# Optimization experiments

Measured on AMD Instinct MI355X. Metric: run time of the kernel, lower is better.

Reference implementation:

```python
import jax, jax.numpy as jnp
import numpy as np

D_IN = 1024
D_OUT = 1024


def setup_inputs() -> dict:
    key = jax.random.key(0)
    kx, kq, kk, kv = jax.random.split(key, 4)
    x = jax.random.normal(kx, (4, 2048, D_IN), dtype=jnp.float32)
    # nn.Linear weight has shape [d_out, d_in]; y = x @ W.T
    s = 1.0 / np.sqrt(D_IN)
    W_query = jax.random.uniform(kq, (D_OUT, D_IN), jnp.float32, -s, s)
    W_key = jax.random.uniform(kk, (D_OUT, D_IN), jnp.float32, -s, s)
    W_value = jax.random.uniform(kv, (D_OUT, D_IN), jnp.float32, -s, s)
    return {"x": x, "W_query": W_query, "W_key": W_key, "W_value": W_value}


def reference(x, W_query, W_key, W_value):
    # x: [b, n, d_in]; W_*: [d_out, d_in]
    q = jnp.einsum("bnd,kd->bnk", x, W_query)
    k = jnp.einsum("bnd,kd->bnk", x, W_key)
    v = jnp.einsum("bnd,kd->bnk", x, W_value)
    d_k = W_query.shape[0]
    scores = jnp.einsum("bqk,bnk->bqn", q, k) * (d_k ** -0.5)  # [b, n, n]
    weights = jax.nn.softmax(scores, axis=-1)
    return jnp.einsum("bqn,bnk->bqk", weights, v)
```

## Files before the change

kernel.cpp:

```cpp
#include <hip/hip_runtime.h>
#include <hip/hip_bf16.h>
#include <stdint.h>


typedef __attribute__((ext_vector_type(8))) short bf16x8;
typedef __attribute__((ext_vector_type(4))) float f32x4;

__device__ __forceinline__ void async_copy16(const void* g, void* l) {
  __builtin_amdgcn_global_load_lds(
      (__attribute__((address_space(1))) void*)(g),
      (__attribute__((address_space(3))) void*)(l),
      16, 0, 0);
}

__device__ __forceinline__ void mainloop256(
    const __hip_bfloat16* __restrict__ aS,
    const __hip_bfloat16* __restrict__ bS,
    __hip_bfloat16* As, __hip_bfloat16* Bs,
    const int wid, const int wm, const int wn,
    const int l16, const int quad, const int sw,
    f32x4 (&acc)[8][4])
{
  const bf16x8* Av = (const bf16x8*)As;
  const bf16x8* Bv = (const bf16x8*)Bs;
  char* lA = (char*)As + wid * 1024;
  char* lB = (char*)Bs + wid * 1024;
  bf16x8 bfr[4][2];
  bf16x8 afc[2][2], afn[2][2];

#define SB0 __builtin_amdgcn_sched_barrier(0)

#define STG_A2(t) do { \
    async_copy16(aS + ((t)*64 +        0), lA + ((t)&1)*32768 +        0); \
    async_copy16(aS + ((t)*64 +  64*1024), lA + ((t)&1)*32768 +  64*128); \
    async_copy16(aS + ((t)*64 + 128*1024), lA + ((t)&1)*32768 + 128*128); \
    async_copy16(aS + ((t)*64 + 192*1024), lA + ((t)&1)*32768 + 192*128); \
  } while (0)
#define STG_B2(t) do { \
    async_copy16(bS + ((t)*64 +        0), lB + ((t)&1)*32768 +        0); \
    async_copy16(bS + ((t)*64 +  64*1024), lB + ((t)&1)*32768 +  64*128); \
    async_copy16(bS + ((t)*64 + 128*1024), lB + ((t)&1)*32768 + 128*128); \
    async_copy16(bS + ((t)*64 + 192*1024), lB + ((t)&1)*32768 + 192*128); \
  } while (0)

#define RD_AF(dst, t, phi) do { \
    _Pragma("unroll") \
    for (int m2 = 0; m2 < 2; ++m2) \
      _Pragma("unroll") \
      for (int kk = 0; kk < 2; ++kk) \
        dst[m2][kk] = Av[((t)&1)*2048 + (wm + ((phi)*2 + m2)*16 + l16)*8 + ((kk*4 + quad) ^ sw)]; \
  } while (0)
#define RD_BF(t, nlo, nhi) do { \
    _Pragma("unroll") \
    for (int ni = (nlo); ni < (nhi); ++ni) \
      _Pragma("unroll") \
      for (int kk = 0; kk < 2; ++kk) \
        bfr[ni][kk] = Bv[((t)&1)*2048 + (wn + ni*16 + l16)*8 + ((kk*4 + quad) ^ sw)]; \
  } while (0)
#define MM(src, phi, nlo, nhi) do { \
    _Pragma("unroll") \
    for (int kk = 0; kk < 2; ++kk) \
      _Pragma("unroll") \
      for (int m2 = 0; m2 < 2; ++m2) \
        _Pragma("unroll") \
        for (int ni = (nlo); ni < (nhi); ++ni) \
          acc[(phi)*2 + m2][ni] = __builtin_amdgcn_mfma_f32_16x16x32_bf16( \
              src[m2][kk], bfr[ni][kk], acc[(phi)*2 + m2][ni], 0, 0, 0); \
  } while (0)

#define TILE(t, STG0_STMT, STG1_STMT, GATE_STMT) do { \
     \
    RD_BF(t, 0, 2); \
    RD_AF(afc, t, 0); \
    STG0_STMT; \
    asm volatile("s_waitcnt lgkmcnt(0)"); SB0; \
    RD_BF(t, 2, 4); \
    SB0; \
    RD_AF(afn, t, 1); \
    SB0; \
    __builtin_amdgcn_s_setprio(1); MM(afc, 0, 0, 2); __builtin_amdgcn_s_setprio(0); \
    asm volatile("s_waitcnt lgkmcnt(4)"); SB0; \
    __builtin_amdgcn_s_setprio(1); MM(afc, 0, 2, 4); __builtin_amdgcn_s_setprio(0); \
    SB0; \
    __builtin_amdgcn_s_barrier();    \
     \
    STG1_STMT; \
    asm volatile("s_waitcnt lgkmcnt(0)"); SB0; \
    RD_AF(afc, t, 2); \
    SB0; \
    __builtin_amdgcn_s_setprio(1); MM(afn, 1, 0, 4); __builtin_amdgcn_s_setprio(0); \
     \
    asm volatile("s_waitcnt lgkmcnt(0)"); SB0; \
    RD_AF(afn, t, 3); \
    SB0; \
    __builtin_amdgcn_s_setprio(1); MM(afc, 2, 0, 4); __builtin_amdgcn_s_setprio(0); \
     \
    asm volatile("s_waitcnt lgkmcnt(0)"); SB0; \
    __builtin_amdgcn_s_setprio(1); MM(afn, 3, 0, 4); __builtin_amdgcn_s_setprio(0); \
    GATE_STMT; \
    SB0; \
    __builtin_amdgcn_s_barrier(); \
  } while (0)

#define GATE4 asm volatile("s_waitcnt vmcnt(4)")
#define GATE0 asm volatile("s_waitcnt vmcnt(0)")
#define GNONE (void)0

  STG_B2(0); STG_A2(0); STG_B2(1);
  asm volatile("s_waitcnt vmcnt(4)");
  __builtin_amdgcn_s_barrier();

  #pragma unroll 1
  for (int i = 0; i < 7; ++i) {
    const int ta = 2 * i, tb = 2 * i + 1;
    TILE(ta, STG_A2(tb),     STG_B2(ta + 2), GATE4);
    TILE(tb, STG_A2(ta + 2), STG_B2(tb + 2), GATE4);
  }
  TILE(14, STG_A2(15), GNONE, GATE0);
  TILE(15, GNONE,      GNONE, GNONE);

#undef TILE
#undef GATE4
#undef GATE0
#undef GNONE
#undef MM
#undef RD_BF
#undef RD_AF
#undef STG_A2
#undef STG_B2
#undef SB0
}

__global__ __launch_bounds__(512, 2)
void gemm_qkv(const __hip_bfloat16* __restrict__ A,
              const __hip_bfloat16* __restrict__ B,
              __hip_bfloat16* __restrict__ Q,
              __hip_bfloat16* __restrict__ Kk,
              __hip_bfloat16* __restrict__ Vt)
{
  __shared__ __align__(16) __hip_bfloat16 As[2][256 * 64];
  __shared__ __align__(16) __hip_bfloat16 Bs[2][256 * 64];

  const int bid = blockIdx.x;
  const int s   = (bid & 7) * 48 + (bid >> 3);
  const long long tile_m = (long long)(s / 12) * 256;
  const long long tile_n = (long long)(s % 12) * 256;

  const int tid  = threadIdx.x;
  const int wid  = tid >> 6;
  const int lane = tid & 63;
  const int srow = wid * 8 + (lane >> 3);
  const int scol = ((lane & 7) ^ (lane >> 3)) * 8;

  const __hip_bfloat16* aS = A + (tile_m + srow) * 1024 + scol;
  const __hip_bfloat16* bS = B + (tile_n + srow) * 1024 + scol;

  const int wm   = (wid >> 2) * 128;
  const int wn   = (wid & 3) * 64;
  const int quad = lane >> 4;
  const int l16  = lane & 15;
  const int sw   = l16 & 7;

  f32x4 acc[8][4];
  #pragma unroll
  for (int mi = 0; mi < 8; ++mi)
    #pragma unroll
    for (int ni = 0; ni < 4; ++ni)
      acc[mi][ni] = (f32x4){0.f, 0.f, 0.f, 0.f};

  mainloop256(aS, bS, &As[0][0], &Bs[0][0], wid, wm, wn, l16, quad, sw, acc);

  const int mat = (int)(tile_n >> 10);
  if (mat < 2) {
    __hip_bfloat16* outp = (mat == 0) ? Q : Kk;
    const float scale = (mat == 0) ? 0.03125f : 1.0f;
    const int coln0 = (int)(tile_n & 1023);
    #pragma unroll
    for (int mi = 0; mi < 8; ++mi) {
      #pragma unroll
      for (int r = 0; r < 4; ++r) {
        const long long row = tile_m + wm + mi * 16 + quad * 4 + r;
        #pragma unroll
        for (int ni = 0; ni < 4; ++ni) {
          const int col = coln0 + wn + ni * 16 + l16;
          outp[row * 1024 + col] = __float2bfloat16(acc[mi][ni][r] * scale);
        }
      }
    }
  } else {
    const int b    = (int)(tile_m >> 11);
    const int seq0 = (int)(tile_m & 2047);
    const int d0   = (int)(tile_n - 2048);
    #pragma unroll
    for (int mi = 0; mi < 8; ++mi) {
      const int seq = seq0 + wm + mi * 16 + quad * 4;
      #pragma unroll
      for (int ni = 0; ni < 4; ++ni) {
        const int d = d0 + wn + ni * 16 + l16;
        union { ushort4 u; unsigned short sh[4]; } pk;
        #pragma unroll
        for (int r = 0; r < 4; ++r)
          pk.sh[r] = __bfloat16_as_ushort(__float2bfloat16(acc[mi][ni][r]));
        *(ushort4*)(Vt + ((long long)(b * 1024 + d)) * 2048 + seq) = pk.u;
      }
    }
  }
}

__global__ __launch_bounds__(512, 2)
void gemm_s_exp(const __hip_bfloat16* __restrict__ A,
                const __hip_bfloat16* __restrict__ B,
                __hip_bfloat16* __restrict__ Cout,
                float* __restrict__ part)
{
  __shared__ __align__(16) __hip_bfloat16 As[2][256 * 64];
  __shared__ __align__(16) __hip_bfloat16 Bs[2][256 * 64];

  const int bz = blockIdx.z;
  A += (long long)bz * 2048 * 1024;
  B += (long long)bz * 2048 * 1024;

  const long long tile_m = (long long)blockIdx.y * 256;
  const long long tile_n = (long long)blockIdx.x * 256;

  const int tid  = threadIdx.x;
  const int wid  = tid >> 6;
  const int lane = tid & 63;
  const int srow = wid * 8 + (lane >> 3);
  const int scol = ((lane & 7) ^ (lane >> 3)) * 8;

  const __hip_bfloat16* aS = A + (tile_m + srow) * 1024 + scol;
  const __hip_bfloat16* bS = B + (tile_n + srow) * 1024 + scol;

  const int wm   = (wid >> 2) * 128;
  const int wn   = (wid & 3) * 64;
  const int quad = lane >> 4;
  const int l16  = lane & 15;
  const int sw   = l16 & 7;

  f32x4 acc[8][4];
  #pragma unroll
  for (int mi = 0; mi < 8; ++mi)
    #pragma unroll
    for (int ni = 0; ni < 4; ++ni)
      acc[mi][ni] = (f32x4){0.f, 0.f, 0.f, 0.f};

  mainloop256(aS, bS, &As[0][0], &Bs[0][0], wid, wm, wn, l16, quad, sw, acc);

  __hip_bfloat16* C = Cout + (long long)bz * 2048 * 2048;
  #pragma unroll
  for (int mi = 0; mi < 8; ++mi) {
    #pragma unroll
    for (int r = 0; r < 4; ++r) {
      const long long row = tile_m + wm + mi * 16 + quad * 4 + r;
      float ssum = 0.f;
      #pragma unroll
      for (int ni = 0; ni < 4; ++ni) {
        const float e = __expf(acc[mi][ni][r]);
        const __hip_bfloat16 h = __float2bfloat16(e);
        C[row * 2048 + tile_n + wn + ni * 16 + l16] = h;
        ssum += __bfloat162float(h);
      }
      #pragma unroll
      for (int off = 1; off < 16; off <<= 1) ssum += __shfl_xor(ssum, off, 64);
      if (l16 == 0)
        part[((long long)bz * 2048 + row) * 32 + blockIdx.x * 4 + (wid & 3)] = ssum;
    }
  }
}

__global__ __launch_bounds__(256)
void gemm_pv(const __hip_bfloat16* __restrict__ A,
             const __hip_bfloat16* __restrict__ B,
             const float* __restrict__ part,
             float* __restrict__ Cout)
{
  __shared__ __align__(16) __hip_bfloat16 As[128 * 64];
  __shared__ __align__(16) __hip_bfloat16 Bs[128 * 64];
  __shared__ float rinv[128];

  const int K = 2048, N = 1024;
  const int bz = blockIdx.z;
  A += (long long)bz * 2048 * 2048;
  B += (long long)bz * 1024 * 2048;

  const long long tile_m = (long long)blockIdx.y * 128;
  const long long tile_n = (long long)blockIdx.x * 128;

  const int tid  = threadIdx.x;
  const int wid  = tid >> 6;
  const int lane = tid & 63;

  const int srow = wid * 8 + (lane >> 3);
  const int scol = (((lane & 7) ^ (lane >> 3))) * 8;

  const __hip_bfloat16* aptr = A + (tile_m + srow) * K + scol;
  const __hip_bfloat16* bptr = B + (tile_n + srow) * K + scol;
  char* la = (char*)As + (wid * 8) * 128;
  char* lb = (char*)Bs + (wid * 8) * 128;

  const int wm   = (wid >> 1) * 64;
  const int wn   = (wid & 1) * 64;
  const int quad = lane >> 4;
  const int l16  = lane & 15;
  const int sw   = l16 & 7;

  const bf16x8* Asv = (const bf16x8*)As;
  const bf16x8* Bsv = (const bf16x8*)Bs;

  f32x4 acc[4][4];
  #pragma unroll
  for (int mi = 0; mi < 4; ++mi)
    #pragma unroll
    for (int ni = 0; ni < 4; ++ni)
      acc[mi][ni] = (f32x4){0.f, 0.f, 0.f, 0.f};

  for (int k0 = 0; k0 < K; k0 += 64) {
    #pragma unroll
    for (int p = 0; p < 4; ++p)
      async_copy16(aptr + (long long)p * 32 * K, la + p * 32 * 128);
    #pragma unroll
    for (int p = 0; p < 4; ++p)
      async_copy16(bptr + (long long)p * 32 * K, lb + p * 32 * 128);
    aptr += 64;
    bptr += 64;
    __syncthreads();

    #pragma unroll
    for (int kk = 0; kk < 2; ++kk) {
      bf16x8 af[4], bfr[4];
      const int ch = (kk * 4 + quad);
      #pragma unroll
      for (int mi = 0; mi < 4; ++mi) af[mi]  = Asv[(wm + mi * 16 + l16) * 8 + (ch ^ sw)];
      #pragma unroll
      for (int ni = 0; ni < 4; ++ni) bfr[ni] = Bsv[(wn + ni * 16 + l16) * 8 + (ch ^ sw)];
      #pragma unroll
      for (int mi = 0; mi < 4; ++mi)
        #pragma unroll
        for (int ni = 0; ni < 4; ++ni)
          acc[mi][ni] = __builtin_amdgcn_mfma_f32_16x16x32_bf16(af[mi], bfr[ni], acc[mi][ni], 0, 0, 0);
    }
    __syncthreads();
  }

  if (tid < 128) {
    const float4* pp = (const float4*)(part + ((long long)bz * 2048 + tile_m + tid) * 32);
    float s = 0.f;
    #pragma unroll
    for (int j = 0; j < 8; ++j) {
      const float4 f = pp[j];
      s += f.x + f.y + f.z + f.w;
    }
    rinv[tid] = 1.f / s;
  }
  __syncthreads();

  float* C = Cout + (long long)bz * 2048 * 1024;
  #pragma unroll
  for (int mi = 0; mi < 4; ++mi) {
    #pragma unroll
    for (int r = 0; r < 4; ++r) {
      const int rloc = wm + mi * 16 + quad * 4 + r;
      const float inv = rinv[rloc];
      const long long row = tile_m + rloc;
      #pragma unroll
      for (int ni = 0; ni < 4; ++ni) {
        const long long col = tile_n + wn + ni * 16 + l16;
        C[row * N + col] = acc[mi][ni][r] * inv;
      }
    }
  }
}

__global__ __launch_bounds__(256)
void cast_all(const float* __restrict__ x,
              const float* __restrict__ Wq, const float* __restrict__ Wk,
              const float* __restrict__ Wv,
              __hip_bfloat16* __restrict__ xb, __hip_bfloat16* __restrict__ wcat)
{
  const int bx = blockIdx.x;
  const float* src;
  __hip_bfloat16* dst;
  int i;
  if (bx < 8192) {
    src = x; dst = xb; i = bx * 256 + threadIdx.x;
  } else {
    const int which = (bx - 8192) >> 10;
    src = (which == 0) ? Wq : (which == 1) ? Wk : Wv;
    dst = wcat + (long long)which * 1048576;
    i = ((bx - 8192) & 1023) * 256 + threadIdx.x;
  }
  const float4 f = ((const float4*)src)[i];
  union { ushort4 u; __hip_bfloat16 h[4]; } r;
  r.h[0] = __float2bfloat16(f.x);
  r.h[1] = __float2bfloat16(f.y);
  r.h[2] = __float2bfloat16(f.z);
  r.h[3] = __float2bfloat16(f.w);
  ((ushort4*)dst)[i] = r.u;
}

extern "C" void kernel_launch(void* const* d_in, const int* in_sizes, int n_in,
                              void* d_out, int out_size, void* d_ws, size_t ws_size,
                              hipStream_t stream)
{
  (void)in_sizes; (void)n_in; (void)out_size; (void)ws_size;

  const float* x  = (const float*)d_in[0];
  const float* Wq = (const float*)d_in[1];
  const float* Wk = (const float*)d_in[2];
  const float* Wv = (const float*)d_in[3];
  float* out = (float*)d_out;

  char* ws = (char*)d_ws;
  __hip_bfloat16* xb   = (__hip_bfloat16*)(ws);
  float*          part = (float*)(ws);
  __hip_bfloat16* wcat = (__hip_bfloat16*)(ws + (16LL << 20));
  __hip_bfloat16* Q    = (__hip_bfloat16*)(ws + (22LL << 20));
  __hip_bfloat16* Kk   = (__hip_bfloat16*)(ws + (38LL << 20));
  __hip_bfloat16* Vt   = (__hip_bfloat16*)(ws + (54LL << 20));
  __hip_bfloat16* S    = (__hip_bfloat16*)(ws + (70LL << 20));

  cast_all<<<11264, 256, 0, stream>>>(x, Wq, Wk, Wv, xb, wcat);

  gemm_qkv<<<dim3(384, 1, 1), 512, 0, stream>>>(xb, wcat, Q, Kk, Vt);

  gemm_s_exp<<<dim3(8, 8, 4), 512, 0, stream>>>(Q, Kk, S, part);

  gemm_pv<<<dim3(8, 16, 4), 256, 0, stream>>>(S, Vt, part, out);
}
```

Baseline: 236.4 us.

## Template the pipelined GEMM mainloop and reuse it for V projection and PV

The 256x256 double-buffered mainloop is templated on N-subtile count, tile count and K stride. The QKV projection is split into a QK kernel with 256x256 tiles and a separate V kernel with 256x128 tiles. The simple single-buffered 128x128 PV GEMM is replaced by the pipelined 256x128 mainloop with 512 threads. The aim is better MFMA pipelining and wave balance on the PV and V GEMMs, at the cost of an extra kernel launch and a 256-block grid for PV.

```diff
diff --git a/kernel.cpp b/kernel.cpp
--- a/kernel.cpp
+++ b/kernel.cpp
@@ -13,34 +13,36 @@
       16, 0, 0);
 }
 
+template<int NI, int NT, int KS>
 __device__ __forceinline__ void mainloop256(
     const __hip_bfloat16* __restrict__ aS,
     const __hip_bfloat16* __restrict__ bS,
     __hip_bfloat16* As, __hip_bfloat16* Bs,
     const int wid, const int wm, const int wn,
     const int l16, const int quad, const int sw,
-    f32x4 (&acc)[8][4])
-{
+    f32x4 (&acc)[8][NI])
+{
+  constexpr int NI2 = NI / 2;
   const bf16x8* Av = (const bf16x8*)As;
   const bf16x8* Bv = (const bf16x8*)Bs;
   char* lA = (char*)As + wid * 1024;
   char* lB = (char*)Bs + wid * 1024;
-  bf16x8 bfr[4][2];
+  bf16x8 bfr[NI][2];
   bf16x8 afc[2][2], afn[2][2];
 
 #define SB0 __builtin_amdgcn_sched_barrier(0)
 
 #define STG_A2(t) do { \
-    async_copy16(aS + ((t)*64 +        0), lA + ((t)&1)*32768 +        0); \
-    async_copy16(aS + ((t)*64 +  64*1024), lA + ((t)&1)*32768 +  64*128); \
-    async_copy16(aS + ((t)*64 + 128*1024), lA + ((t)&1)*32768 + 128*128); \
-    async_copy16(aS + ((t)*64 + 192*1024), lA + ((t)&1)*32768 + 192*128); \
+    _Pragma("unroll") \
+    for (int p = 0; p < 4; ++p) \
+      async_copy16(aS + ((t)*64 + (long long)p * 64 * KS), \
+                   lA + ((t)&1)*32768 + p * 64 * 128); \
   } while (0)
 #define STG_B2(t) do { \
-    async_copy16(bS + ((t)*64 +        0), lB + ((t)&1)*32768 +        0); \
-    async_copy16(bS + ((t)*64 +  64*1024), lB + ((t)&1)*32768 +  64*128); \
-    async_copy16(bS + ((t)*64 + 128*1024), lB + ((t)&1)*32768 + 128*128); \
-    async_copy16(bS + ((t)*64 + 192*1024), lB + ((t)&1)*32768 + 192*128); \
+    _Pragma("unroll") \
+    for (int p = 0; p < NI; ++p) \
+      async_copy16(bS + ((t)*64 + (long long)p * 64 * KS), \
+                   lB + ((t)&1)*(NI*8192) + p * 64 * 128); \
   } while (0)
 
 #define RD_AF(dst, t, phi) do { \
@@ -55,7 +57,7 @@
     for (int ni = (nlo); ni < (nhi); ++ni) \
       _Pragma("unroll") \
       for (int kk = 0; kk < 2; ++kk) \
-        bfr[ni][kk] = Bv[((t)&1)*2048 + (wn + ni*16 + l16)*8 + ((kk*4 + quad) ^ sw)]; \
+        bfr[ni][kk] = Bv[((t)&1)*(NI*512) + (wn + ni*16 + l16)*8 + ((kk*4 + quad) ^ sw)]; \
   } while (0)
 #define MM(src, phi, nlo, nhi) do { \
     _Pragma("unroll") \
@@ -70,17 +72,17 @@
 
 #define TILE(t, STG0_STMT, STG1_STMT, GATE_STMT) do { \
      \
-    RD_BF(t, 0, 2); \
+    RD_BF(t, 0, NI2); \
     RD_AF(afc, t, 0); \
     STG0_STMT; \
     asm volatile("s_waitcnt lgkmcnt(0)"); SB0; \
-    RD_BF(t, 2, 4); \
+    RD_BF(t, NI2, NI); \
     SB0; \
     RD_AF(afn, t, 1); \
     SB0; \
-    __builtin_amdgcn_s_setprio(1); MM(afc, 0, 0, 2); __builtin_amdgcn_s_setprio(0); \
+    __builtin_amdgcn_s_setprio(1); MM(afc, 0, 0, NI2); __builtin_amdgcn_s_setprio(0); \
     asm volatile("s_waitcnt lgkmcnt(4)"); SB0; \
-    __builtin_amdgcn_s_setprio(1); MM(afc, 0, 2, 4); __builtin_amdgcn_s_setprio(0); \
+    __builtin_amdgcn_s_setprio(1); MM(afc, 0, NI2, NI); __builtin_amdgcn_s_setprio(0); \
     SB0; \
     __builtin_amdgcn_s_barrier();    \
      \
@@ -88,39 +90,40 @@
     asm volatile("s_waitcnt lgkmcnt(0)"); SB0; \
     RD_AF(afc, t, 2); \
     SB0; \
-    __builtin_amdgcn_s_setprio(1); MM(afn, 1, 0, 4); __builtin_amdgcn_s_setprio(0); \
+    __builtin_amdgcn_s_setprio(1); MM(afn, 1, 0, NI); __builtin_amdgcn_s_setprio(0); \
      \
     asm volatile("s_waitcnt lgkmcnt(0)"); SB0; \
     RD_AF(afn, t, 3); \
     SB0; \
-    __builtin_amdgcn_s_setprio(1); MM(afc, 2, 0, 4); __builtin_amdgcn_s_setprio(0); \
+    __builtin_amdgcn_s_setprio(1); MM(afc, 2, 0, NI); __builtin_amdgcn_s_setprio(0); \
      \
     asm volatile("s_waitcnt lgkmcnt(0)"); SB0; \
-    __builtin_amdgcn_s_setprio(1); MM(afn, 3, 0, 4); __builtin_amdgcn_s_setprio(0); \
+    __builtin_amdgcn_s_setprio(1); MM(afn, 3, 0, NI); __builtin_amdgcn_s_setprio(0); \
     GATE_STMT; \
     SB0; \
     __builtin_amdgcn_s_barrier(); \
   } while (0)
 
-#define GATE4 asm volatile("s_waitcnt vmcnt(4)")
+#define GATEN do { if constexpr (NI == 4) asm volatile("s_waitcnt vmcnt(4)"); \
+                   else                   asm volatile("s_waitcnt vmcnt(2)"); } while (0)
 #define GATE0 asm volatile("s_waitcnt vmcnt(0)")
 #define GNONE (void)0
 
   STG_B2(0); STG_A2(0); STG_B2(1);
-  asm volatile("s_waitcnt vmcnt(4)");
+  GATEN;
   __builtin_amdgcn_s_barrier();
 
   #pragma unroll 1
-  for (int i = 0; i < 7; ++i) {
+  for (int i = 0; i < NT / 2 - 1; ++i) {
     const int ta = 2 * i, tb = 2 * i + 1;
-    TILE(ta, STG_A2(tb),     STG_B2(ta + 2), GATE4);
-    TILE(tb, STG_A2(ta + 2), STG_B2(tb + 2), GATE4);
-  }
-  TILE(14, STG_A2(15), GNONE, GATE0);
-  TILE(15, GNONE,      GNONE, GNONE);
+    TILE(ta, STG_A2(tb),     STG_B2(ta + 2), GATEN);
+    TILE(tb, STG_A2(ta + 2), STG_B2(tb + 2), GATEN);
+  }
+  TILE(NT - 2, STG_A2(NT - 1), GNONE, GATE0);
+  TILE(NT - 1, GNONE,          GNONE, GNONE);
 
 #undef TILE
-#undef GATE4
+#undef GATEN
 #undef GATE0
 #undef GNONE
 #undef MM
@@ -132,19 +135,18 @@
 }
 
 __global__ __launch_bounds__(512, 2)
-void gemm_qkv(const __hip_bfloat16* __restrict__ A,
-              const __hip_bfloat16* __restrict__ B,
-              __hip_bfloat16* __restrict__ Q,
-              __hip_bfloat16* __restrict__ Kk,
-              __hip_bfloat16* __restrict__ Vt)
+void gemm_qk(const __hip_bfloat16* __restrict__ A,
+             const __hip_bfloat16* __restrict__ B,
+             __hip_bfloat16* __restrict__ Q,
+             __hip_bfloat16* __restrict__ Kk)
 {
   __shared__ __align__(16) __hip_bfloat16 As[2][256 * 64];
   __shared__ __align__(16) __hip_bfloat16 Bs[2][256 * 64];
 
   const int bid = blockIdx.x;
-  const int s   = (bid & 7) * 48 + (bid >> 3);
-  const long long tile_m = (long long)(s / 12) * 256;
-  const long long tile_n = (long long)(s % 12) * 256;
+  const int s   = (bid & 7) * 32 + (bid >> 3);
+  const long long tile_m = (long long)(s >> 3) * 256;
+  const long long tile_n = (long long)(s & 7) * 256;
 
   const int tid  = threadIdx.x;
   const int wid  = tid >> 6;
@@ -168,41 +170,79 @@
     for (int ni = 0; ni < 4; ++ni)
       acc[mi][ni] = (f32x4){0.f, 0.f, 0.f, 0.f};
 
-  mainloop256(aS, bS, &As[0][0], &Bs[0][0], wid, wm, wn, l16, quad, sw, acc);
+  mainloop256<4, 16, 1024>(aS, bS, &As[0][0], &Bs[0][0],
+                           wid, wm, wn, l16, quad, sw, acc);
 
   const int mat = (int)(tile_n >> 10);
-  if (mat < 2) {
-    __hip_bfloat16* outp = (mat == 0) ? Q : Kk;
-    const float scale = (mat == 0) ? 0.03125f : 1.0f;
-    const int coln0 = (int)(tile_n & 1023);
-    #pragma unroll
-    for (int mi = 0; mi < 8; ++mi) {
+  __hip_bfloat16* outp = (mat == 0) ? Q : Kk;
+  const float scale = (mat == 0) ? 0.03125f : 1.0f;
+  const int coln0 = (int)(tile_n & 1023);
+  #pragma unroll
+  for (int mi = 0; mi < 8; ++mi) {
+    #pragma unroll
+    for (int r = 0; r < 4; ++r) {
+      const long long row = tile_m + wm + mi * 16 + quad * 4 + r;
       #pragma unroll
-      for (int r = 0; r < 4; ++r) {
-        const long long row = tile_m + wm + mi * 16 + quad * 4 + r;
-        #pragma unroll
-        for (int ni = 0; ni < 4; ++ni) {
-          const int col = coln0 + wn + ni * 16 + l16;
-          outp[row * 1024 + col] = __float2bfloat16(acc[mi][ni][r] * scale);
-        }
+      for (int ni = 0; ni < 4; ++ni) {
+        const int col = coln0 + wn + ni * 16 + l16;
+        outp[row * 1024 + col] = __float2bfloat16(acc[mi][ni][r] * scale);
       }
     }
-  } else {
-    const int b    = (int)(tile_m >> 11);
-    const int seq0 = (int)(tile_m & 2047);
-    const int d0   = (int)(tile_n - 2048);
-    #pragma unroll
-    for (int mi = 0; mi < 8; ++mi) {
-      const int seq = seq0 + wm + mi * 16 + quad * 4;
+  }
+}
+
+__global__ __launch_bounds__(512, 2)
+void gemm_v(const __hip_bfloat16* __restrict__ A,
+            const __hip_bfloat16* __restrict__ B,
+            __hip_bfloat16* __restrict__ Vt)
+{
+  __shared__ __align__(16) __hip_bfloat16 As[2][256 * 64];
+  __shared__ __align__(16) __hip_bfloat16 Bs[2][128 * 64];
+
+  const int bid = blockIdx.x;
+  const int s   = (bid & 7) * 32 + (bid >> 3);
+  const long long tile_m = (long long)(s >> 3) * 256;
+  const long long tile_n = (long long)(s & 7) * 128;
+
+  const int tid  = threadIdx.x;
+  const int wid  = tid >> 6;
+  const int lane = tid & 63;
+  const int srow = wid * 8 + (lane >> 3);
+  const int scol = ((lane & 7) ^ (lane >> 3)) * 8;
+
+  const __hip_bfloat16* aS = A + (tile_m + srow) * 1024 + scol;
+  const __hip_bfloat16* bS = B + (tile_n + srow) * 1024 + scol;
+
+  const int wm   = (wid >> 2) * 128;
+  const int wn   = (wid & 3) * 32;
+  const int quad = lane >> 4;
+  const int l16  = lane & 15;
+  const int sw   = l16 & 7;
+
+  f32x4 acc[8][2];
+  #pragma unroll
+  for (int mi = 0; mi < 8; ++mi)
+    #pragma unroll
+    for (int ni = 0; ni < 2; ++ni)
+      acc[mi][ni] = (f32x4){0.f, 0.f, 0.f, 0.f};
+
+  mainloop256<2, 16, 1024>(aS, bS, &As[0][0], &Bs[0][0],
+                           wid, wm, wn, l16, quad, sw, acc);
+
+  const int b    = (int)(tile_m >> 11);
+  const int seq0 = (int)(tile_m & 2047);
+  const int d0   = (int)tile_n;
+  #pragma unroll
+  for (int mi = 0; mi < 8; ++mi) {
+    const int seq = seq0 + wm + mi * 16 + quad * 4;
+    #pragma unroll
+    for (int ni = 0; ni < 2; ++ni) {
+      const int d = d0 + wn + ni * 16 + l16;
+      union { ushort4 u; unsigned short sh[4]; } pk;
       #pragma unroll
-      for (int ni = 0; ni < 4; ++ni) {
-        const int d = d0 + wn + ni * 16 + l16;
-        union { ushort4 u; unsigned short sh[4]; } pk;
-        #pragma unroll
-        for (int r = 0; r < 4; ++r)
-          pk.sh[r] = __bfloat16_as_ushort(__float2bfloat16(acc[mi][ni][r]));
-        *(ushort4*)(Vt + ((long long)(b * 1024 + d)) * 2048 + seq) = pk.u;
-      }
+      for (int r = 0; r < 4; ++r)
+        pk.sh[r] = __bfloat16_as_ushort(__float2bfloat16(acc[mi][ni][r]));
+      *(ushort4*)(Vt + ((long long)(b * 1024 + d)) * 2048 + seq) = pk.u;
     }
   }
 }
@@ -245,7 +285,8 @@
     for (int ni = 0; ni < 4; ++ni)
       acc[mi][ni] = (f32x4){0.f, 0.f, 0.f, 0.f};
 
-  mainloop256(aS, bS, &As[0][0], &Bs[0][0], wid, wm, wn, l16, quad, sw, acc);
+  mainloop256<4, 16, 1024>(aS, bS, &As[0][0], &Bs[0][0],
+                           wid, wm, wn, l16, quad, sw, acc);
 
   __hip_bfloat16* C = Cout + (long long)bz * 2048 * 2048;
   #pragma unroll
@@ -269,81 +310,49 @@
   }
 }
 
-__global__ __launch_bounds__(256)
+__global__ __launch_bounds__(512, 2)
 void gemm_pv(const __hip_bfloat16* __restrict__ A,
              const __hip_bfloat16* __restrict__ B,
              const float* __restrict__ part,
              float* __restrict__ Cout)
 {
-  __shared__ __align__(16) __hip_bfloat16 As[128 * 64];
-  __shared__ __align__(16) __hip_bfloat16 Bs[128 * 64];
-  __shared__ float rinv[128];
-
-  const int K = 2048, N = 1024;
+  __shared__ __align__(16) __hip_bfloat16 As[2][256 * 64];
+  __shared__ __align__(16) __hip_bfloat16 Bs[2][128 * 64];
+  __shared__ float rinv[256];
+
   const int bz = blockIdx.z;
   A += (long long)bz * 2048 * 2048;
   B += (long long)bz * 1024 * 2048;
 
-  const long long tile_m = (long long)blockIdx.y * 128;
+  const long long tile_m = (long long)blockIdx.y * 256;
   const long long tile_n = (long long)blockIdx.x * 128;
 
   const int tid  = threadIdx.x;
   const int wid  = tid >> 6;
   const int lane = tid & 63;
-
   const int srow = wid * 8 + (lane >> 3);
-  const int scol = (((lane & 7) ^ (lane >> 3))) * 8;
-
-  const __hip_bfloat16* aptr = A + (tile_m + srow) * K + scol;
-  const __hip_bfloat16* bptr = B + (tile_n + srow) * K + scol;
-  char* la = (char*)As + (wid * 8) * 128;
-  char* lb = (char*)Bs + (wid * 8) * 128;
-
-  const int wm   = (wid >> 1) * 64;
-  const int wn   = (wid & 1) * 64;
+  const int scol = ((lane & 7) ^ (lane >> 3)) * 8;
+
+  const __hip_bfloat16* aS = A + (tile_m + srow) * 2048 + scol;
+  const __hip_bfloat16* bS = B + (tile_n + srow) * 2048 + scol;
+
+  const int wm   = (wid >> 2) * 128;
+  const int wn   = (wid & 3) * 32;
   const int quad = lane >> 4;
   const int l16  = lane & 15;
   const int sw   = l16 & 7;
 
-  const bf16x8* Asv = (const bf16x8*)As;
-  const bf16x8* Bsv = (const bf16x8*)Bs;
-
-  f32x4 acc[4][4];
-  #pragma unroll
-  for (int mi = 0; mi < 4; ++mi)
-    #pragma unroll
-    for (int ni = 0; ni < 4; ++ni)
+  f32x4 acc[8][2];
+  #pragma unroll
+  for (int mi = 0; mi < 8; ++mi)
+    #pragma unroll
+    for (int ni = 0; ni < 2; ++ni)
       acc[mi][ni] = (f32x4){0.f, 0.f, 0.f, 0.f};
 
-  for (int k0 = 0; k0 < K; k0 += 64) {
-    #pragma unroll
-    for (int p = 0; p < 4; ++p)
-      async_copy16(aptr + (long long)p * 32 * K, la + p * 32 * 128);
-    #pragma unroll
-    for (int p = 0; p < 4; ++p)
-      async_copy16(bptr + (long long)p * 32 * K, lb + p * 32 * 128);
-    aptr += 64;
-    bptr += 64;
-    __syncthreads();
-
-    #pragma unroll
-    for (int kk = 0; kk < 2; ++kk) {
-      bf16x8 af[4], bfr[4];
-      const int ch = (kk * 4 + quad);
-      #pragma unroll
-      for (int mi = 0; mi < 4; ++mi) af[mi]  = Asv[(wm + mi * 16 + l16) * 8 + (ch ^ sw)];
-      #pragma unroll
-      for (int ni = 0; ni < 4; ++ni) bfr[ni] = Bsv[(wn + ni * 16 + l16) * 8 + (ch ^ sw)];
-      #pragma unroll
-      for (int mi = 0; mi < 4; ++mi)
-        #pragma unroll
-        for (int ni = 0; ni < 4; ++ni)
-          acc[mi][ni] = __builtin_amdgcn_mfma_f32_16x16x32_bf16(af[mi], bfr[ni], acc[mi][ni], 0, 0, 0);
-    }
-    __syncthreads();
-  }
-
-  if (tid < 128) {
+  mainloop256<2, 32, 2048>(aS, bS, &As[0][0], &Bs[0][0],
+                           wid, wm, wn, l16, quad, sw, acc);
+
+  if (tid < 256) {
     const float4* pp = (const float4*)(part + ((long long)bz * 2048 + tile_m + tid) * 32);
     float s = 0.f;
     #pragma unroll
@@ -357,16 +366,16 @@
 
   float* C = Cout + (long long)bz * 2048 * 1024;
   #pragma unroll
-  for (int mi = 0; mi < 4; ++mi) {
+  for (int mi = 0; mi < 8; ++mi) {
     #pragma unroll
     for (int r = 0; r < 4; ++r) {
       const int rloc = wm + mi * 16 + quad * 4 + r;
       const float inv = rinv[rloc];
       const long long row = tile_m + rloc;
       #pragma unroll
-      for (int ni = 0; ni < 4; ++ni) {
+      for (int ni = 0; ni < 2; ++ni) {
         const long long col = tile_n + wn + ni * 16 + l16;
-        C[row * N + col] = acc[mi][ni][r] * inv;
+        C[row * 1024 + col] = acc[mi][ni][r] * inv;
       }
     }
   }
@@ -422,9 +431,11 @@
 
   cast_all<<<11264, 256, 0, stream>>>(x, Wq, Wk, Wv, xb, wcat);
 
-  gemm_qkv<<<dim3(384, 1, 1), 512, 0, stream>>>(xb, wcat, Q, Kk, Vt);
+  gemm_qk<<<256, 512, 0, stream>>>(xb, wcat, Q, Kk);
+
+  gemm_v<<<256, 512, 0, stream>>>(xb, wcat + 2097152, Vt);
 
   gemm_s_exp<<<dim3(8, 8, 4), 512, 0, stream>>>(Q, Kk, S, part);
 
-  gemm_pv<<<dim3(8, 16, 4), 256, 0, stream>>>(S, Vt, part, out);
-}
+  gemm_pv<<<dim3(8, 8, 4), 512, 0, stream>>>(S, Vt, part, out);
+}
```

Result: no change. 234.3 us (-0.9%).
